# Kernel optimization log

Measured on AMD Instinct MI355X. Metric: run time of the kernel, lower is better.

Reference implementation:

```python
import jax, jax.numpy as jnp
import numpy as np

H = 8          # num_heads (in_channels > 8)
BN_EPS = 1e-5  # torch BatchNorm2d default


def _l2norm(w):
    # torch.norm(w, 2, dim=-2, keepdim=True) + 1e-4
    return jnp.sqrt(jnp.sum(w * w, axis=-2, keepdims=True)) + 1e-4


def setup_inputs() -> dict:
    key = jax.random.key(0)
    ks = jax.random.split(key, 6)
    N, C, T, V = 64, 128, 128, 25
    x = jax.random.normal(ks[0], (N, C, T, V), dtype=jnp.float32)
    fc1 = jax.random.normal(ks[1], (3, H, V, V), dtype=jnp.float32)
    rpe = jax.random.normal(ks[2], (3, H, V), dtype=jnp.float32)
    hops = jax.random.randint(ks[3], (V, V), 0, V)
    fc2_w = jax.random.normal(ks[4], (3, C, C // H), dtype=jnp.float32) * 0.1
    fc2_b = jax.random.normal(ks[5], (3, C), dtype=jnp.float32) * 0.1
    gamma = jnp.ones((C,), dtype=jnp.float32)
    beta = jnp.zeros((C,), dtype=jnp.float32)
    return {"x": x, "fc1": fc1, "rpe": rpe, "hops": hops,
            "fc2_w": fc2_w, "fc2_b": fc2_b, "gamma": gamma, "beta": beta}


def reference(x, fc1, rpe, hops, fc2_w, fc2_b, gamma, beta):
    N, C, T, V = x.shape
    c = C // H
    # relative-position embedding gathered by hop distance: (3, H, V, V)
    pos_emb = rpe[:, :, hops]
    x_in = x.reshape(N, H, c, T, V)
    y = jnp.zeros((N, H, c, T, V), dtype=x.dtype)
    for i in range(3):
        # normalized adaptive adjacency + normalized positional term
        w1 = fc1[i] / _l2norm(fc1[i]) + pos_emb[i] / _l2norm(pos_emb[i])  # (H, V, V)
        z = jnp.einsum('nhctv,hvw->nhctw', x_in, w1)
        # grouped 1x1 conv == per-head channel mixing
        wg = fc2_w[i].reshape(H, c, c)                       # (H, out_per_group, in_per_group)
        z = jnp.einsum('nhctv,hdc->nhdtv', z, wg)
        z = z + fc2_b[i].reshape(1, H, c, 1, 1)
        y = y + z
    y = y.reshape(N, C, T, V)
    # BatchNorm2d (training-mode batch statistics, biased variance)
    mean = jnp.mean(y, axis=(0, 2, 3), keepdims=True)
    var = jnp.var(y, axis=(0, 2, 3), keepdims=True)
    y = gamma.reshape(1, C, 1, 1) * (y - mean) * jax.lax.rsqrt(var + BN_EPS) + beta.reshape(1, C, 1, 1)
    # residual (in_channels == out_channels -> identity down) + ReLU
    return jax.nn.relu(y + x)
```

## Files before the change

kernel.cpp:

```cpp
#include <hip/hip_runtime.h>
#include <hip/hip_bf16.h>

namespace {

constexpr int kN = 64, kC = 128, kT = 128, kV = 25, kH = 8, kc = 16;
constexpr int kKS = 13;
constexpr int kBCol = 448;
constexpr int kBStep = kBCol * 32;
constexpr int kXRow = 416;

typedef __attribute__((ext_vector_type(8))) short bf16x8;
typedef __attribute__((ext_vector_type(8))) unsigned short u16x8;
typedef __attribute__((ext_vector_type(4))) float f32x4;

__device__ inline unsigned short f2bf(float f) {
    unsigned int u = __builtin_bit_cast(unsigned int, f);
    u += 0x7fffu + ((u >> 16) & 1u);
    return (unsigned short)(u >> 16);
}
__device__ inline float bf2f(unsigned short s) {
    return __builtin_bit_cast(float, ((unsigned int)s) << 16);
}
__device__ inline void glds16(const void* g, void* l) {
    __builtin_amdgcn_global_load_lds(
        (const __attribute__((address_space(1))) void*)g,
        (__attribute__((address_space(3))) void*)l, 16, 0, 0);
}

#define VMWAIT0() do { asm volatile("s_waitcnt vmcnt(0)" ::: "memory"); \
                       __builtin_amdgcn_sched_barrier(0); } while (0)
#define LGKM0()   do { asm volatile("s_waitcnt lgkmcnt(0)" ::: "memory"); \
                       __builtin_amdgcn_sched_barrier(0); } while (0)
#define BAR()     __builtin_amdgcn_s_barrier()

__global__ void precompute_w1(const float* __restrict__ fc1,
                              const float* __restrict__ rpe,
                              const int* __restrict__ hops,
                              float* __restrict__ W1) {
    int ih = blockIdx.x;
    int w = threadIdx.x;
    if (w >= kV) return;
    const float* f = fc1 + ih * kV * kV;
    const float* r = rpe + ih * kV;
    float s1 = 0.f, s2 = 0.f;
    for (int v = 0; v < kV; ++v) {
        float a = f[v * kV + w];
        float p = r[hops[v * kV + w]];
        s1 += a * a; s2 += p * p;
    }
    float n1 = sqrtf(s1) + 1e-4f, n2 = sqrtf(s2) + 1e-4f;
    float* o = W1 + ih * kV * kV;
    for (int v = 0; v < kV; ++v) {
        float a = f[v * kV + w];
        float p = r[hops[v * kV + w]];
        o[v * kV + w] = a / n1 + p / n2;
    }
}

__global__ void precompute_W(const float* __restrict__ W1,
                             const float* __restrict__ fc2_w,
                             unsigned short* __restrict__ Wt3) {
    int k = blockIdx.x;
    int h = blockIdx.y;
    unsigned short* outp = Wt3 + ((size_t)h * kKS + k) * kBStep;
    for (int e = threadIdx.x; e < kBStep; e += 256) {
        int col = e >> 5, lo = e & 31;
        int kap = k * 32 + lo;
        int c = kap / 26, vv = kap - c * 26;
        float val = 0.f;
        if (vv < 25 && col < 400) {
            int d = col / 25, w = col - d * 25;
            #pragma unroll
            for (int i = 0; i < 3; ++i) {
                float wg = fc2_w[(i * kC + h * kc + d) * kc + c];
                float w1 = W1[((i * kH + h) * kV + vv) * kV + w];
                val += wg * w1;
            }
        }
        outp[e] = f2bf(val);
    }
}

__global__ __launch_bounds__(256, 2) void gemm_y(const float* __restrict__ x,
                                                 const unsigned short* __restrict__ Wt3,
                                                 unsigned short* __restrict__ yb,
                                                 float2* __restrict__ Pbuf) {
    __shared__ __align__(16) unsigned short Xl[64 * kXRow];
    __shared__ __align__(16) unsigned short Bl[kBStep];

    const int tb = blockIdx.x, n = blockIdx.y, h = blockIdx.z;
    const int tid = threadIdx.x, lane = tid & 63, wv = tid >> 6;
    const int ll = lane & 15, lh = lane >> 4;
    const int t0 = tb * 64;

    const float* xbase = x + ((size_t)(n * kC + h * kc) * kT + t0) * kV;
    const unsigned short* bbase = Wt3 + (size_t)h * kKS * kBStep;
    float* Blf = (float*)&Bl[0];

    auto stage_x = [&](int s) {
        #pragma unroll
        for (int q = 0; q < 7; ++q) {
            int e = q * 256 + tid;
            if (e < 1600) {
                int c = e / 400, off = e - c * 400;
                glds16(xbase + (size_t)(s * 4 + c) * 3200 + off * 4,
                       (char*)Bl + (size_t)e * 16);
            }
        }
    };
    auto stage_b = [&](int k) {
        const unsigned short* src = bbase + (size_t)k * kBStep;
        #pragma unroll
        for (int q = 0; q < 7; ++q) {
            int e = q * 256 + tid;
            glds16(src + (size_t)e * 8, Bl + (size_t)e * 8);
        }
    };
    auto convert = [&](int s) {
        const int t = lane;
        const int t13 = t % 13;
        const float* bp = Blf + wv * 1600 + t * 25;
        unsigned int* xw = (unsigned int*)&Xl[0] + t * (kXRow / 2) + (s * 4 + wv) * 13;
        #pragma unroll
        for (int i = 0; i < 13; ++i) {
            int p = i + t13; if (p >= 13) p -= 13;
            float f0 = bp[2 * p];
            float f1 = (p < 12) ? bp[2 * p + 1] : 0.f;
            xw[p] = (unsigned)f2bf(f0) | ((unsigned)f2bf(f1) << 16);
        }
    };

    #pragma unroll 1
    for (int s = 0; s < 4; ++s) {
        stage_x(s);
        VMWAIT0(); BAR();
        convert(s);
        LGKM0(); BAR();
    }
    stage_b(0);

    f32x4 acc[4][7];
    #pragma unroll
    for (int a = 0; a < 4; ++a)
        #pragma unroll
        for (int b = 0; b < 7; ++b) acc[a][b] = (f32x4)(0.f);

    #pragma unroll 1
    for (int k = 0; k < kKS; ++k) {
        VMWAIT0();
        BAR();

        bf16x8 a0 = *(const bf16x8*)&Xl[(size_t)(0 * 16 + ll) * kXRow + k * 32 + lh * 8];
        bf16x8 a1 = *(const bf16x8*)&Xl[(size_t)(1 * 16 + ll) * kXRow + k * 32 + lh * 8];
        bf16x8 a2 = *(const bf16x8*)&Xl[(size_t)(2 * 16 + ll) * kXRow + k * 32 + lh * 8];
        bf16x8 a3 = *(const bf16x8*)&Xl[(size_t)(3 * 16 + ll) * kXRow + k * 32 + lh * 8];
        bf16x8 b[7];
        #pragma unroll
        for (int ci = 0; ci < 7; ++ci)
            b[ci] = *(const bf16x8*)&Bl[(size_t)((wv * 7 + ci) * 16 + ll) * 32 + lh * 8];

        LGKM0(); BAR();
        if (k < kKS - 1) stage_b(k + 1);

        #pragma unroll
        for (int ci = 0; ci < 7; ++ci) {
            acc[0][ci] = __builtin_amdgcn_mfma_f32_16x16x32_bf16(a0, b[ci], acc[0][ci], 0, 0, 0);
            acc[1][ci] = __builtin_amdgcn_mfma_f32_16x16x32_bf16(a1, b[ci], acc[1][ci], 0, 0, 0);
            acc[2][ci] = __builtin_amdgcn_mfma_f32_16x16x32_bf16(a2, b[ci], acc[2][ci], 0, 0, 0);
            acc[3][ci] = __builtin_amdgcn_mfma_f32_16x16x32_bf16(a3, b[ci], acc[3][ci], 0, 0, 0);
        }
    }

    #pragma unroll
    for (int rf = 0; rf < 4; ++rf) {
        int t = t0 + rf * 16 + lh * 4;
        #pragma unroll
        for (int ci = 0; ci < 7; ++ci) {
            int m = wv * 112 + ci * 16 + ll;
            if (m < 400) {
                int d = m / 25, w = m - d * 25;
                unsigned short* yp = yb + ((size_t)(n * kC + h * kc + d) * kT + t) * kV + w;
                #pragma unroll
                for (int r = 0; r < 4; ++r)
                    yp[(size_t)r * kV] = f2bf(acc[rf][ci][r]);
            }
        }
    }

    float2* Bs = (float2*)&Bl[0];
    #pragma unroll
    for (int ci = 0; ci < 7; ++ci) {
        float s = 0.f, ss = 0.f;
        #pragma unroll
        for (int rf = 0; rf < 4; ++rf)
            #pragma unroll
            for (int r = 0; r < 4; ++r) {
                float v = acc[rf][ci][r];
                s += v; ss += v * v;
            }
        s  += __shfl_xor(s, 16);  ss += __shfl_xor(ss, 16);
        s  += __shfl_xor(s, 32);  ss += __shfl_xor(ss, 32);
        if (lh == 0) Bs[wv * 112 + ci * 16 + ll] = make_float2(s, ss);
    }
    __syncthreads();
    if (tid < 16) {
        float s = 0.f, ss = 0.f;
        for (int w = 0; w < 25; ++w) {
            float2 p = Bs[tid * 25 + w];
            s += p.x; ss += p.y;
        }
        size_t bid = (size_t)tb + 2 * ((size_t)n + 64 * (size_t)h);
        Pbuf[bid * 16 + tid] = make_float2(s, ss);
    }
}

__global__ void bn_finalize(const float2* __restrict__ Pbuf,
                            const float* __restrict__ gamma,
                            const float* __restrict__ beta,
                            float2* __restrict__ scsh) {
    int ch = threadIdx.x;
    if (ch >= kC) return;
    int h = ch >> 4, d = ch & 15;
    float s = 0.f, ss = 0.f;
    for (int j = 0; j < 128; ++j) {
        float2 p = Pbuf[(size_t)(j + 128 * h) * 16 + d];
        s += p.x; ss += p.y;
    }
    const float inv = 1.f / (float)(kN * kT * kV);
    float mean = s * inv;
    float var  = ss * inv - mean * mean;
    float sc = gamma[ch] * rsqrtf(var + 1e-5f);
    scsh[ch] = make_float2(sc, beta[ch] - mean * sc);
}

__global__ void bn_apply(const unsigned short* __restrict__ yb,
                         const float* __restrict__ x,
                         const float2* __restrict__ scsh,
                         float* __restrict__ out) {
    const size_t total8 = (size_t)kN * kC * kT * kV / 8;
    for (size_t i = (size_t)blockIdx.x * blockDim.x + threadIdx.x; i < total8;
         i += (size_t)gridDim.x * blockDim.x) {
        int ch = (int)((i / 400) % kC);
        float2 sc = scsh[ch];
        u16x8 yv = ((const u16x8*)yb)[i];
        f32x4 x0 = ((const f32x4*)x)[i * 2];
        f32x4 x1 = ((const f32x4*)x)[i * 2 + 1];
        f32x4 o0, o1;
        #pragma unroll
        for (int q = 0; q < 4; ++q) {
            o0[q] = fmaxf(bf2f((unsigned short)yv[q]) * sc.x + sc.y + x0[q], 0.f);
            o1[q] = fmaxf(bf2f((unsigned short)yv[q + 4]) * sc.x + sc.y + x1[q], 0.f);
        }
        ((f32x4*)out)[i * 2]     = o0;
        ((f32x4*)out)[i * 2 + 1] = o1;
    }
}

}

extern "C" void kernel_launch(void* const* d_in, const int* in_sizes, int n_in,
                              void* d_out, int out_size, void* d_ws, size_t ws_size,
                              hipStream_t stream) {
    const float* x     = (const float*)d_in[0];
    const float* fc1   = (const float*)d_in[1];
    const float* rpe   = (const float*)d_in[2];
    const int*   hops  = (const int*)d_in[3];
    const float* fc2w  = (const float*)d_in[4];
    const float* gamma = (const float*)d_in[6];
    const float* beta  = (const float*)d_in[7];
    float* out = (float*)d_out;

    char* ws = (char*)d_ws;
    unsigned short* yb   = (unsigned short*)ws;
    float*          W1   = (float*)(ws + 52428800);
    unsigned short* Wt3  = (unsigned short*)(ws + 52494336);
    float2*         Pbuf = (float2*)(ws + 55476224);
    float2*         scsh = (float2*)(ws + 55607296);

    precompute_w1<<<24, 32, 0, stream>>>(fc1, rpe, hops, W1);
    precompute_W<<<dim3(13, 8), 256, 0, stream>>>(W1, fc2w, Wt3);
    gemm_y<<<dim3(2, 64, 8), 256, 0, stream>>>(x, Wt3, yb, Pbuf);
    bn_finalize<<<1, 128, 0, stream>>>(Pbuf, gamma, beta, scsh);
    bn_apply<<<2048, 256, 0, stream>>>(yb, x, scsh, out);
}
```

Baseline: 131.3 us.

## Load GEMM B fragments directly from global into registers with double buffering

```diff
diff --git a/kernel.cpp b/kernel.cpp
--- a/kernel.cpp
+++ b/kernel.cpp
@@ -26,12 +26,6 @@
         (const __attribute__((address_space(1))) void*)g,
         (__attribute__((address_space(3))) void*)l, 16, 0, 0);
 }
-
-#define VMWAIT0() do { asm volatile("s_waitcnt vmcnt(0)" ::: "memory"); \
-                       __builtin_amdgcn_sched_barrier(0); } while (0)
-#define LGKM0()   do { asm volatile("s_waitcnt lgkmcnt(0)" ::: "memory"); \
-                       __builtin_amdgcn_sched_barrier(0); } while (0)
-#define BAR()     __builtin_amdgcn_s_barrier()
 
 __global__ void precompute_w1(const float* __restrict__ fc1,
                               const float* __restrict__ rpe,
@@ -86,7 +80,7 @@
                                                  unsigned short* __restrict__ yb,
                                                  float2* __restrict__ Pbuf) {
     __shared__ __align__(16) unsigned short Xl[64 * kXRow];
-    __shared__ __align__(16) unsigned short Bl[kBStep];
+    __shared__ __align__(16) float bounce[6400];
 
     const int tb = blockIdx.x, n = blockIdx.y, h = blockIdx.z;
     const int tid = threadIdx.x, lane = tid & 63, wv = tid >> 6;
@@ -94,82 +88,73 @@
     const int t0 = tb * 64;
 
     const float* xbase = x + ((size_t)(n * kC + h * kc) * kT + t0) * kV;
-    const unsigned short* bbase = Wt3 + (size_t)h * kKS * kBStep;
-    float* Blf = (float*)&Bl[0];
-
-    auto stage_x = [&](int s) {
+    const unsigned short* bbase = Wt3 + (size_t)h * kKS * kBStep
+                                + ((size_t)(wv * 7) * 16 + ll) * 32 + lh * 8;
+
+    for (int s = 0; s < 4; ++s) {
         #pragma unroll
         for (int q = 0; q < 7; ++q) {
             int e = q * 256 + tid;
             if (e < 1600) {
                 int c = e / 400, off = e - c * 400;
                 glds16(xbase + (size_t)(s * 4 + c) * 3200 + off * 4,
-                       (char*)Bl + (size_t)e * 16);
-            }
-        }
+                       (char*)bounce + (size_t)e * 16);
+            }
+        }
+        __syncthreads();
+        {
+            const int t = lane, t13 = t % 13;
+            const float* bp = bounce + wv * 1600 + t * 25;
+            unsigned int* xw = (unsigned int*)&Xl[0] + t * (kXRow / 2) + (s * 4 + wv) * 13;
+            #pragma unroll
+            for (int i = 0; i < 13; ++i) {
+                int p = i + t13; if (p >= 13) p -= 13;
+                float f0 = bp[2 * p];
+                float f1 = (p < 12) ? bp[2 * p + 1] : 0.f;
+                xw[p] = (unsigned)f2bf(f0) | ((unsigned)f2bf(f1) << 16);
+            }
+        }
+        __syncthreads();
+    }
+
+    f32x4 acc[4][7];
+    #pragma unroll
+    for (int a = 0; a < 4; ++a)
+        #pragma unroll
+        for (int b = 0; b < 7; ++b) acc[a][b] = (f32x4)(0.f);
+
+    auto bld = [&](int k, int ci) -> bf16x8 {
+        return *(const bf16x8*)(bbase + (size_t)k * kBStep + ci * 512);
     };
-    auto stage_b = [&](int k) {
-        const unsigned short* src = bbase + (size_t)k * kBStep;
-        #pragma unroll
-        for (int q = 0; q < 7; ++q) {
-            int e = q * 256 + tid;
-            glds16(src + (size_t)e * 8, Bl + (size_t)e * 8);
-        }
-    };
-    auto convert = [&](int s) {
-        const int t = lane;
-        const int t13 = t % 13;
-        const float* bp = Blf + wv * 1600 + t * 25;
-        unsigned int* xw = (unsigned int*)&Xl[0] + t * (kXRow / 2) + (s * 4 + wv) * 13;
-        #pragma unroll
-        for (int i = 0; i < 13; ++i) {
-            int p = i + t13; if (p >= 13) p -= 13;
-            float f0 = bp[2 * p];
-            float f1 = (p < 12) ? bp[2 * p + 1] : 0.f;
-            xw[p] = (unsigned)f2bf(f0) | ((unsigned)f2bf(f1) << 16);
-        }
-    };
-
-    #pragma unroll 1
-    for (int s = 0; s < 4; ++s) {
-        stage_x(s);
-        VMWAIT0(); BAR();
-        convert(s);
-        LGKM0(); BAR();
-    }
-    stage_b(0);
-
-    f32x4 acc[4][7];
-    #pragma unroll
-    for (int a = 0; a < 4; ++a)
-        #pragma unroll
-        for (int b = 0; b < 7; ++b) acc[a][b] = (f32x4)(0.f);
-
-    #pragma unroll 1
-    for (int k = 0; k < kKS; ++k) {
-        VMWAIT0();
-        BAR();
-
+    auto amfma = [&](int k, bf16x8* bf) {
         bf16x8 a0 = *(const bf16x8*)&Xl[(size_t)(0 * 16 + ll) * kXRow + k * 32 + lh * 8];
         bf16x8 a1 = *(const bf16x8*)&Xl[(size_t)(1 * 16 + ll) * kXRow + k * 32 + lh * 8];
         bf16x8 a2 = *(const bf16x8*)&Xl[(size_t)(2 * 16 + ll) * kXRow + k * 32 + lh * 8];
         bf16x8 a3 = *(const bf16x8*)&Xl[(size_t)(3 * 16 + ll) * kXRow + k * 32 + lh * 8];
-        bf16x8 b[7];
-        #pragma unroll
-        for (int ci = 0; ci < 7; ++ci)
-            b[ci] = *(const bf16x8*)&Bl[(size_t)((wv * 7 + ci) * 16 + ll) * 32 + lh * 8];
-
-        LGKM0(); BAR();
-        if (k < kKS - 1) stage_b(k + 1);
-
         #pragma unroll
         for (int ci = 0; ci < 7; ++ci) {
-            acc[0][ci] = __builtin_amdgcn_mfma_f32_16x16x32_bf16(a0, b[ci], acc[0][ci], 0, 0, 0);
-            acc[1][ci] = __builtin_amdgcn_mfma_f32_16x16x32_bf16(a1, b[ci], acc[1][ci], 0, 0, 0);
-            acc[2][ci] = __builtin_amdgcn_mfma_f32_16x16x32_bf16(a2, b[ci], acc[2][ci], 0, 0, 0);
-            acc[3][ci] = __builtin_amdgcn_mfma_f32_16x16x32_bf16(a3, b[ci], acc[3][ci], 0, 0, 0);
-        }
-    }
+            acc[0][ci] = __builtin_amdgcn_mfma_f32_16x16x32_bf16(a0, bf[ci], acc[0][ci], 0, 0, 0);
+            acc[1][ci] = __builtin_amdgcn_mfma_f32_16x16x32_bf16(a1, bf[ci], acc[1][ci], 0, 0, 0);
+            acc[2][ci] = __builtin_amdgcn_mfma_f32_16x16x32_bf16(a2, bf[ci], acc[2][ci], 0, 0, 0);
+            acc[3][ci] = __builtin_amdgcn_mfma_f32_16x16x32_bf16(a3, bf[ci], acc[3][ci], 0, 0, 0);
+        }
+    };
+
+    bf16x8 bA[7], bB[7];
+    #pragma unroll
+    for (int ci = 0; ci < 7; ++ci) bA[ci] = bld(0, ci);
+
+    int k = 0;
+    #pragma unroll 1
+    for (int it = 0; it < 6; ++it, k += 2) {
+        #pragma unroll
+        for (int ci = 0; ci < 7; ++ci) bB[ci] = bld(k + 1, ci);
+        amfma(k, bA);
+        #pragma unroll
+        for (int ci = 0; ci < 7; ++ci) bA[ci] = bld(k + 2, ci);
+        amfma(k + 1, bB);
+    }
+    amfma(12, bA);
 
     #pragma unroll
     for (int rf = 0; rf < 4; ++rf) {
@@ -187,7 +172,7 @@
         }
     }
 
-    float2* Bs = (float2*)&Bl[0];
+    float2* Bs = (float2*)&bounce[0];
     #pragma unroll
     for (int ci = 0; ci < 7; ++ci) {
         float s = 0.f, ss = 0.f;
```

Measured after the change: 134.0 us. 1.02x slower.
